# Optimization experiments

Measured on AMD Instinct MI355X. Metric: run time of the kernel, lower is better.

## Reference

```python
import jax, jax.numpy as jnp
import numpy as np

B, C, H, W = 8, 64, 64, 64   # C == embed_dim
NUM_EMBED = 8192
BETA = 0.25


def setup_inputs() -> dict:
    key = jax.random.key(0)
    k1, k2 = jax.random.split(key)
    z = jax.random.normal(k1, (B, C, H, W), dtype=jnp.float32)
    # nn.Embedding init: uniform(-1/num_embed, 1/num_embed)
    embedding = jax.random.uniform(
        k2, (NUM_EMBED, C), minval=-1.0 / NUM_EMBED, maxval=1.0 / NUM_EMBED,
        dtype=jnp.float32)
    return {"z": z, "embedding": embedding}


def reference(z, embedding):
    beta = BETA
    num_embed, embed_dim = embedding.shape
    eps = 1e-10

    zc = jnp.transpose(z, (0, 2, 3, 1))            # b h w c
    zf = zc.reshape(-1, embed_dim)                 # [N, d]

    # cosine distance: normalize both (z detached in torch; argmax is
    # non-differentiable anyway)
    zn = jax.lax.stop_gradient(
        zf / jnp.linalg.norm(zf, axis=1, keepdims=True))
    en = embedding / jnp.linalg.norm(embedding, axis=1, keepdims=True)
    d = jnp.einsum('bd,nd->bn', zn, en)            # [N, K] similarity

    # sort(dim=1) then take last column == argmax
    encoding_indices = jnp.argmax(d, axis=1)       # [N]

    # one-hot @ codebook == gather (same math)
    z_q = jnp.take(embedding, encoding_indices, axis=0).reshape(zc.shape)

    sg = jax.lax.stop_gradient
    loss = beta * jnp.mean((sg(z_q) - zc) ** 2) + jnp.mean((z_q - sg(zc)) ** 2)

    # straight-through estimator, back to b c h w
    z_q_st = zc + sg(z_q - zc)
    out = jnp.transpose(z_q_st, (0, 3, 1, 2))

    # perplexity from one-hot usage histogram
    n_tok = encoding_indices.shape[0]
    avg_probs = jnp.zeros((num_embed,), dtype=d.dtype).at[encoding_indices].add(1.0) / n_tok
    perplexity = jnp.exp(-jnp.sum(avg_probs * jnp.log(avg_probs + eps)))

    idx_map = encoding_indices.reshape(z.shape[0], 1, z.shape[2], z.shape[3])
    return out, loss, perplexity, idx_map
```

## Files before the change

kernel.cpp:

```cpp
#include <hip/hip_runtime.h>
#include <hip/hip_bf16.h>
#include <math.h>

#define B_    8
#define C_    64
#define H_    64
#define W_    64
#define NUM_EMBED 8192
#define DIMS  64
#define N_TOK (B_ * H_ * W_)
#define N_ELEM (B_ * C_ * H_ * W_)

typedef short v8s __attribute__((ext_vector_type(8)));
typedef float v4f __attribute__((ext_vector_type(4)));

#define MARGIN 0.011f

__device__ __forceinline__ short bf16_rne(float x) {
    unsigned u = __float_as_uint(x);
    unsigned r = (u + 0x7FFFu + ((u >> 16) & 1u)) >> 16;
    return (short)r;
}
__device__ __forceinline__ unsigned mono(float f) {
    int b = __float_as_int(f);
    return (unsigned)(b ^ ((b >> 31) | 0x80000000));
}
__device__ __forceinline__ float demono(unsigned u) {
    int b = (u >> 31) ? (int)(u ^ 0x80000000u) : (int)~u;
    return __int_as_float(b);
}
__device__ __forceinline__ unsigned long long pack_win(float d, int code) {
    return ((unsigned long long)mono(d) << 32) | (unsigned)(0xFFFFFFFFu - (unsigned)code);
}

__global__ void invnorm_kernel(const float* __restrict__ emb, float* __restrict__ invn) {
    int wave = threadIdx.x >> 6;
    int lane = threadIdx.x & 63;
    int row  = blockIdx.x * 4 + wave;
    float v = emb[row * DIMS + lane];
    float s = v * v;
    #pragma unroll
    for (int off = 1; off < 64; off <<= 1) s += __shfl_xor(s, off, 64);
    if (lane == 0) invn[row] = 1.0f / sqrtf(s);
}

__global__ void en_frag_kernel(const float* __restrict__ emb, const float* __restrict__ invn,
                               v8s* __restrict__ ef) {
    int ch = blockIdx.x * 256 + threadIdx.x;
    int l  = ch & 63;
    int st = (ch >> 6) & 1;
    int ct = ch >> 7;
    int code = ct * 16 + (l & 15);
    int kb   = st * 32 + ((l >> 4) & 3) * 8;
    float rn = invn[code];
    v8s o;
    #pragma unroll
    for (int j = 0; j < 8; ++j) o[j] = bf16_rne(emb[code * DIMS + kb + j] * rn);
    ef[ch] = o;
}

__global__ __launch_bounds__(256)
void z_prep_kernel(const float* __restrict__ z, float* __restrict__ z_tok,
                   v8s* __restrict__ af) {
    __shared__ float zs[64][65];
    __shared__ float part[4][64];
    __shared__ float rn[64];
    const int tid = threadIdx.x;
    const int w   = tid & 63;
    const int cg  = tid >> 6;
    const int bh  = blockIdx.x;
    const int b   = bh >> 6, h = bh & 63;

    const float* zb = z + (size_t)b * (C_ * H_ * W_) + h * W_;
    float ss = 0.f;
    #pragma unroll
    for (int cc = 0; cc < 16; ++cc) {
        int c = cg * 16 + cc;
        float v = zb[c * (H_ * W_) + w];
        zs[c][w] = v;
        ss += v * v;
    }
    part[cg][w] = ss;
    __syncthreads();
    if (tid < 64) {
        float s = part[0][tid] + part[1][tid] + part[2][tid] + part[3][tid];
        rn[tid] = 1.0f / sqrtf(s);
    }
    __syncthreads();

    {
        int c  = tid & 63;
        int tg = tid >> 6;
        #pragma unroll
        for (int i = 0; i < 16; ++i) {
            int tloc = tg * 16 + i;
            z_tok[(size_t)(bh * 64 + tloc) * DIMS + c] = zs[c][tloc];
        }
    }
    #pragma unroll
    for (int ii = 0; ii < 2; ++ii) {
        int ch  = tid + ii * 256;
        int mtl = ch >> 7;
        int st  = (ch >> 6) & 1;
        int l   = ch & 63;
        int tloc = mtl * 16 + (l & 15);
        int kb   = st * 32 + ((l >> 4) & 3) * 8;
        float rr = rn[tloc];
        v8s o;
        #pragma unroll
        for (int j = 0; j < 8; ++j) o[j] = bf16_rne(zs[kb + j][tloc] * rr);
        af[(size_t)((bh * 4 + mtl) * 2 + st) * 64 + l] = o;
    }
}

#define RT 4
#define CHUNK_TILES 16
#define TILES_PER_BLOCK 64
#define CHUNKS (TILES_PER_BLOCK / CHUNK_TILES)

__global__ __launch_bounds__(512, 4)
void pass1_kernel(const v8s* __restrict__ af, const v8s* __restrict__ ef,
                  unsigned* __restrict__ tokmax) {
    __shared__ v8s lds[CHUNK_TILES * 2 * 64];
    const int tid  = threadIdx.x;
    const int lane = tid & 63;
    const int wave = tid >> 6;
    const int bm    = blockIdx.x >> 3;
    const int split = blockIdx.x & 7;
    const int tile0 = split * TILES_PER_BLOCK;

    const int mtb = bm * 32 + wave * RT;
    v8s a[RT][2];
    #pragma unroll
    for (int r = 0; r < RT; ++r)
        #pragma unroll
        for (int s = 0; s < 2; ++s)
            a[r][s] = af[(size_t)((mtb + r) * 2 + s) * 64 + lane];

    v4f mx[RT];
    #pragma unroll
    for (int r = 0; r < RT; ++r) mx[r] = (v4f){-1e30f, -1e30f, -1e30f, -1e30f};

    const float4* gsrc = (const float4*)(ef + (size_t)tile0 * 2 * 64);
    float4* lf = (float4*)lds;
    float4 pre[4];
    #pragma unroll
    for (int i = 0; i < 4; ++i) pre[i] = gsrc[tid + i * 512];

    for (int c = 0; c < CHUNKS; ++c) {
        __syncthreads();
        #pragma unroll
        for (int i = 0; i < 4; ++i) lf[tid + i * 512] = pre[i];
        if (c + 1 < CHUNKS) {
            const float4* nx = gsrc + (size_t)(c + 1) * 2048;
            #pragma unroll
            for (int i = 0; i < 4; ++i) pre[i] = nx[tid + i * 512];
        }
        __syncthreads();
        #pragma unroll
        for (int j = 0; j < CHUNK_TILES; ++j) {
            v8s b0 = lds[(j * 2 + 0) * 64 + lane];
            v8s b1 = lds[(j * 2 + 1) * 64 + lane];
            #pragma unroll
            for (int r = 0; r < RT; ++r) {
                v4f t = (v4f){0.f, 0.f, 0.f, 0.f};
                t = __builtin_amdgcn_mfma_f32_16x16x32_bf16(a[r][0], b0, t, 0, 0, 0);
                t = __builtin_amdgcn_mfma_f32_16x16x32_bf16(a[r][1], b1, t, 0, 0, 0);
                mx[r][0] = fmaxf(mx[r][0], t[0]);
                mx[r][1] = fmaxf(mx[r][1], t[1]);
                mx[r][2] = fmaxf(mx[r][2], t[2]);
                mx[r][3] = fmaxf(mx[r][3], t[3]);
            }
        }
    }
    #pragma unroll
    for (int r = 0; r < RT; ++r)
        #pragma unroll
        for (int i = 0; i < 4; ++i) {
            float v = mx[r][i];
            v = fmaxf(v, __shfl_xor(v, 1, 64));
            v = fmaxf(v, __shfl_xor(v, 2, 64));
            v = fmaxf(v, __shfl_xor(v, 4, 64));
            v = fmaxf(v, __shfl_xor(v, 8, 64));
            mx[r][i] = v;
        }
    if ((lane & 15) == 0) {
        int q = lane >> 4;
        #pragma unroll
        for (int r = 0; r < RT; ++r)
            #pragma unroll
            for (int i = 0; i < 4; ++i) {
                int tok = (mtb + r) * 16 + q * 4 + i;
                atomicMax(&tokmax[tok], mono(mx[r][i]));
            }
    }
}

__global__ __launch_bounds__(512, 4)
void pass2_kernel(const v8s* __restrict__ af, const v8s* __restrict__ ef,
                  const unsigned* __restrict__ tokmax,
                  const float* __restrict__ z_tok, const float* __restrict__ emb,
                  const float* __restrict__ invn,
                  unsigned long long* __restrict__ winner) {
    __shared__ v8s lds[CHUNK_TILES * 2 * 64];
    const int tid  = threadIdx.x;
    const int lane = tid & 63;
    const int wave = tid >> 6;
    const int bm    = blockIdx.x >> 3;
    const int split = blockIdx.x & 7;
    const int tile0 = split * TILES_PER_BLOCK;

    const int mtb = bm * 32 + wave * RT;
    v8s a[RT][2];
    #pragma unroll
    for (int r = 0; r < RT; ++r)
        #pragma unroll
        for (int s = 0; s < 2; ++s)
            a[r][s] = af[(size_t)((mtb + r) * 2 + s) * 64 + lane];

    float thr[RT][4];
    {
        int q = lane >> 4;
        #pragma unroll
        for (int r = 0; r < RT; ++r)
            #pragma unroll
            for (int i = 0; i < 4; ++i)
                thr[r][i] = demono(tokmax[(mtb + r) * 16 + q * 4 + i]) - MARGIN;
    }

    const float4* gsrc = (const float4*)(ef + (size_t)tile0 * 2 * 64);
    float4* lf = (float4*)lds;
    float4 pre[4];
    #pragma unroll
    for (int i = 0; i < 4; ++i) pre[i] = gsrc[tid + i * 512];

    for (int c = 0; c < CHUNKS; ++c) {
        __syncthreads();
        #pragma unroll
        for (int i = 0; i < 4; ++i) lf[tid + i * 512] = pre[i];
        if (c + 1 < CHUNKS) {
            const float4* nx = gsrc + (size_t)(c + 1) * 2048;
            #pragma unroll
            for (int i = 0; i < 4; ++i) pre[i] = nx[tid + i * 512];
        }
        __syncthreads();
        #pragma unroll 4
        for (int j = 0; j < CHUNK_TILES; ++j) {
            v8s b0 = lds[(j * 2 + 0) * 64 + lane];
            v8s b1 = lds[(j * 2 + 1) * 64 + lane];
            v4f acc[RT];
            #pragma unroll
            for (int r = 0; r < RT; ++r) {
                v4f t = (v4f){0.f, 0.f, 0.f, 0.f};
                t = __builtin_amdgcn_mfma_f32_16x16x32_bf16(a[r][0], b0, t, 0, 0, 0);
                t = __builtin_amdgcn_mfma_f32_16x16x32_bf16(a[r][1], b1, t, 0, 0, 0);
                acc[r] = t;
            }
            unsigned pm = 0;
            #pragma unroll
            for (int r = 0; r < RT; ++r)
                #pragma unroll
                for (int i = 0; i < 4; ++i)
                    if (acc[r][i] >= thr[r][i]) pm |= (1u << (r * 4 + i));
            unsigned long long act = __ballot(pm != 0);
            if (act) {
                const int ctile = tile0 + c * CHUNK_TILES + j;
                while (act) {
                    int sl = __ffsll(act) - 1;
                    act &= act - 1;
                    unsigned lm = __shfl(pm, sl, 64);
                    const int code = ctile * 16 + (sl & 15);
                    while (lm) {
                        int bit = __ffs(lm) - 1;
                        lm &= lm - 1;
                        int r = bit >> 2, i = bit & 3;
                        int tok = (mtb + r) * 16 + ((sl >> 4) & 3) * 4 + i;
                        float p = z_tok[(size_t)tok * DIMS + lane] *
                                  emb[(size_t)code * DIMS + lane];
                        #pragma unroll
                        for (int o = 32; o; o >>= 1) p += __shfl_xor(p, o, 64);
                        float d = p * invn[code];
                        if (lane == 0) atomicMax(&winner[tok], pack_win(d, code));
                    }
                }
            }
        }
    }
}

__global__ void fin_idx_kernel(const unsigned long long* __restrict__ winner,
                               int* __restrict__ idx, float* __restrict__ idxmap) {
    int t = blockIdx.x * 256 + threadIdx.x;
    unsigned code = 0xFFFFFFFFu - (unsigned)(winner[t] & 0xFFFFFFFFull);
    idx[t] = (int)code;
    idxmap[t] = (float)code;
}

__global__ void gather_loss_kernel(const float* __restrict__ z,
                                   const float* __restrict__ emb,
                                   const int* __restrict__ idx,
                                   float* __restrict__ out,
                                   float* __restrict__ partial,
                                   int* __restrict__ hist) {
    __shared__ float red[256];
    const int tid  = threadIdx.x;
    const int lane = tid & 63;
    const int wave = tid >> 6;
    const int bt   = blockIdx.x;
    const int b    = bt >> 6;
    const int h    = bt & 63;

    const int t  = bt * 64 + lane;
    const int id = idx[t];
    const long base = (long)b * (C_ * H_ * W_) + h * W_ + lane;

    float sse = 0.f;
    #pragma unroll
    for (int cc = 0; cc < 16; ++cc) {
        const int c = wave * 16 + cc;
        const float q  = emb[id * DIMS + c];
        const float zv = z[base + (long)c * (H_ * W_)];
        out[base + (long)c * (H_ * W_)] = zv + (q - zv);
        const float d = q - zv;
        sse += d * d;
    }

    red[tid] = sse;
    __syncthreads();
    for (int s = 128; s > 0; s >>= 1) {
        if (tid < s) red[tid] += red[tid + s];
        __syncthreads();
    }
    if (tid == 0) partial[bt] = red[0];
    if (wave == 0) atomicAdd(&hist[id], 1);
}

__global__ void finalize_kernel(const float* __restrict__ partial,
                                const int* __restrict__ hist,
                                float* __restrict__ out_scal) {
    __shared__ double red[256];
    const int tid = threadIdx.x;

    double s = 0.0;
    for (int i = tid; i < 512; i += 256) s += (double)partial[i];
    red[tid] = s;
    __syncthreads();
    for (int st = 128; st > 0; st >>= 1) {
        if (tid < st) red[tid] += red[tid + st];
        __syncthreads();
    }
    const double sse = red[0];
    __syncthreads();

    double e = 0.0;
    for (int k = tid; k < NUM_EMBED; k += 256) {
        float p = (float)hist[k] / (float)N_TOK;
        e += (double)(p * logf(p + 1e-10f));
    }
    red[tid] = e;
    __syncthreads();
    for (int st = 128; st > 0; st >>= 1) {
        if (tid < st) red[tid] += red[tid + st];
        __syncthreads();
    }
    if (tid == 0) {
        out_scal[0] = (float)(1.25 * sse / (double)N_ELEM);
        out_scal[1] = expf(-(float)red[0]);
    }
}

extern "C" void kernel_launch(void* const* d_in, const int* in_sizes, int n_in,
                              void* d_out, int out_size, void* d_ws, size_t ws_size,
                              hipStream_t stream) {
    const float* z   = (const float*)d_in[0];
    const float* emb = (const float*)d_in[1];
    float* o = (float*)d_out;

    char* ws = (char*)d_ws;
    v8s*  af      = (v8s*)ws;
    v8s*  ef      = (v8s*)(ws + 4194304);
    unsigned long long* winner = (unsigned long long*)(ws + 5242880);
    unsigned* tokmax = (unsigned*)(ws + 5505024);
    int*   idx     = (int*)(ws + 5636096);
    float* invn    = (float*)(ws + 5767168);
    int*   hist    = (int*)(ws + 5799936);
    float* partial = (float*)(ws + 5832704);

    float* out_q      = o;
    float* out_scal   = o + N_ELEM;
    float* out_idxmap = o + N_ELEM + 2;
    float* z_tok      = o;

    hipMemsetAsync(tokmax, 0, N_TOK * sizeof(unsigned), stream);
    hipMemsetAsync(winner, 0, N_TOK * sizeof(unsigned long long), stream);
    hipMemsetAsync(hist,   0, NUM_EMBED * sizeof(int), stream);

    invnorm_kernel<<<NUM_EMBED / 4, 256, 0, stream>>>(emb, invn);
    en_frag_kernel<<<256, 256, 0, stream>>>(emb, invn, ef);
    z_prep_kernel<<<512, 256, 0, stream>>>(z, z_tok, af);
    pass1_kernel<<<512, 512, 0, stream>>>(af, ef, tokmax);
    pass2_kernel<<<512, 512, 0, stream>>>(af, ef, tokmax, z_tok, emb, invn, winner);
    fin_idx_kernel<<<N_TOK / 256, 256, 0, stream>>>(winner, idx, out_idxmap);
    gather_loss_kernel<<<N_TOK / 64, 256, 0, stream>>>(z, emb, idx, out_q, partial, hist);
    finalize_kernel<<<1, 256, 0, stream>>>(partial, hist, out_scal);
}
```

Baseline: 196.1 us.

## Replace second MFMA pass with per-chunk max bounds and fp32 chunk rescoring

Pass1 now records a rounded-up 16-bit per-chunk maximum similarity for every token across 32 codebook chunks of 256 codes, plus the global max. The second full MFMA sweep over the codebook is replaced by a per-token rescore kernel. It rescans in fp32 only the chunks whose upper bound reaches the threshold, then does an in-wave argmax with lowest-index tie-breaking. This removes a full second GEMM pass, the 64-bit atomics and the finalize-index kernel. The cost is extra cmax writes and scattered fp32 codebook reads for every chunk that qualifies.

```diff
diff --git a/kernel.cpp b/kernel.cpp
--- a/kernel.cpp
+++ b/kernel.cpp
@@ -28,9 +28,6 @@
 __device__ __forceinline__ float demono(unsigned u) {
     int b = (u >> 31) ? (int)(u ^ 0x80000000u) : (int)~u;
     return __int_as_float(b);
-}
-__device__ __forceinline__ unsigned long long pack_win(float d, int code) {
-    return ((unsigned long long)mono(d) << 32) | (unsigned)(0xFFFFFFFFu - (unsigned)code);
 }
 
 __global__ void invnorm_kernel(const float* __restrict__ emb, float* __restrict__ invn) {
@@ -117,10 +114,12 @@
 #define CHUNK_TILES 16
 #define TILES_PER_BLOCK 64
 #define CHUNKS (TILES_PER_BLOCK / CHUNK_TILES)
+#define NCHUNK_TOT 32
 
 __global__ __launch_bounds__(512, 4)
 void pass1_kernel(const v8s* __restrict__ af, const v8s* __restrict__ ef,
-                  unsigned* __restrict__ tokmax) {
+                  unsigned* __restrict__ tokmax,
+                  unsigned short* __restrict__ cmax) {
     __shared__ v8s lds[CHUNK_TILES * 2 * 64];
     const int tid  = threadIdx.x;
     const int lane = tid & 63;
@@ -137,9 +136,9 @@
         for (int s = 0; s < 2; ++s)
             a[r][s] = af[(size_t)((mtb + r) * 2 + s) * 64 + lane];
 
-    v4f mx[RT];
-    #pragma unroll
-    for (int r = 0; r < RT; ++r) mx[r] = (v4f){-1e30f, -1e30f, -1e30f, -1e30f};
+    v4f gm[RT];
+    #pragma unroll
+    for (int r = 0; r < RT; ++r) gm[r] = (v4f){-1e30f, -1e30f, -1e30f, -1e30f};
 
     const float4* gsrc = (const float4*)(ef + (size_t)tile0 * 2 * 64);
     float4* lf = (float4*)lds;
@@ -157,6 +156,11 @@
             for (int i = 0; i < 4; ++i) pre[i] = nx[tid + i * 512];
         }
         __syncthreads();
+
+        v4f mxc[RT];
+        #pragma unroll
+        for (int r = 0; r < RT; ++r) mxc[r] = (v4f){-1e30f, -1e30f, -1e30f, -1e30f};
+
         #pragma unroll
         for (int j = 0; j < CHUNK_TILES; ++j) {
             v8s b0 = lds[(j * 2 + 0) * 64 + lane];
@@ -166,24 +170,39 @@
                 v4f t = (v4f){0.f, 0.f, 0.f, 0.f};
                 t = __builtin_amdgcn_mfma_f32_16x16x32_bf16(a[r][0], b0, t, 0, 0, 0);
                 t = __builtin_amdgcn_mfma_f32_16x16x32_bf16(a[r][1], b1, t, 0, 0, 0);
-                mx[r][0] = fmaxf(mx[r][0], t[0]);
-                mx[r][1] = fmaxf(mx[r][1], t[1]);
-                mx[r][2] = fmaxf(mx[r][2], t[2]);
-                mx[r][3] = fmaxf(mx[r][3], t[3]);
+                mxc[r][0] = fmaxf(mxc[r][0], t[0]);
+                mxc[r][1] = fmaxf(mxc[r][1], t[1]);
+                mxc[r][2] = fmaxf(mxc[r][2], t[2]);
+                mxc[r][3] = fmaxf(mxc[r][3], t[3]);
             }
         }
-    }
-    #pragma unroll
-    for (int r = 0; r < RT; ++r)
-        #pragma unroll
-        for (int i = 0; i < 4; ++i) {
-            float v = mx[r][i];
-            v = fmaxf(v, __shfl_xor(v, 1, 64));
-            v = fmaxf(v, __shfl_xor(v, 2, 64));
-            v = fmaxf(v, __shfl_xor(v, 4, 64));
-            v = fmaxf(v, __shfl_xor(v, 8, 64));
-            mx[r][i] = v;
-        }
+
+        #pragma unroll
+        for (int r = 0; r < RT; ++r)
+            #pragma unroll
+            for (int i = 0; i < 4; ++i) {
+                float v = mxc[r][i];
+                v = fmaxf(v, __shfl_xor(v, 1, 64));
+                v = fmaxf(v, __shfl_xor(v, 2, 64));
+                v = fmaxf(v, __shfl_xor(v, 4, 64));
+                v = fmaxf(v, __shfl_xor(v, 8, 64));
+                mxc[r][i] = v;
+                gm[r][i]  = fmaxf(gm[r][i], v);
+            }
+        if ((lane & 15) == 0) {
+            const int q   = lane >> 4;
+            const int cid = split * CHUNKS + c;
+            #pragma unroll
+            for (int r = 0; r < RT; ++r)
+                #pragma unroll
+                for (int i = 0; i < 4; ++i) {
+                    int tok = (mtb + r) * 16 + q * 4 + i;
+                    cmax[tok * NCHUNK_TOT + cid] =
+                        (unsigned short)((mono(mxc[r][i]) + 0xFFFFu) >> 16);
+                }
+        }
+    }
+
     if ((lane & 15) == 0) {
         int q = lane >> 4;
         #pragma unroll
@@ -191,109 +210,76 @@
             #pragma unroll
             for (int i = 0; i < 4; ++i) {
                 int tok = (mtb + r) * 16 + q * 4 + i;
-                atomicMax(&tokmax[tok], mono(mx[r][i]));
+                atomicMax(&tokmax[tok], mono(gm[r][i]));
             }
     }
 }
 
-__global__ __launch_bounds__(512, 4)
-void pass2_kernel(const v8s* __restrict__ af, const v8s* __restrict__ ef,
-                  const unsigned* __restrict__ tokmax,
-                  const float* __restrict__ z_tok, const float* __restrict__ emb,
-                  const float* __restrict__ invn,
-                  unsigned long long* __restrict__ winner) {
-    __shared__ v8s lds[CHUNK_TILES * 2 * 64];
-    const int tid  = threadIdx.x;
-    const int lane = tid & 63;
-    const int wave = tid >> 6;
-    const int bm    = blockIdx.x >> 3;
-    const int split = blockIdx.x & 7;
-    const int tile0 = split * TILES_PER_BLOCK;
-
-    const int mtb = bm * 32 + wave * RT;
-    v8s a[RT][2];
-    #pragma unroll
-    for (int r = 0; r < RT; ++r)
-        #pragma unroll
-        for (int s = 0; s < 2; ++s)
-            a[r][s] = af[(size_t)((mtb + r) * 2 + s) * 64 + lane];
-
-    float thr[RT][4];
+__global__ __launch_bounds__(256)
+void rescore_kernel(const unsigned short* __restrict__ cmax,
+                    const unsigned* __restrict__ tokmax,
+                    const float* __restrict__ z_tok,
+                    const float* __restrict__ emb,
+                    const float* __restrict__ invn,
+                    int* __restrict__ idx, float* __restrict__ idxmap) {
+    __shared__ float zsh[4][64];
+    const int tid   = threadIdx.x;
+    const int lane  = tid & 63;
+    const int wave  = tid >> 6;
+    const int token = blockIdx.x * 4 + wave;
+
+    zsh[wave][lane] = z_tok[(size_t)token * DIMS + lane];
+    __syncthreads();
+
+    float4 zr[16];
     {
-        int q = lane >> 4;
-        #pragma unroll
-        for (int r = 0; r < RT; ++r)
-            #pragma unroll
-            for (int i = 0; i < 4; ++i)
-                thr[r][i] = demono(tokmax[(mtb + r) * 16 + q * 4 + i]) - MARGIN;
-    }
-
-    const float4* gsrc = (const float4*)(ef + (size_t)tile0 * 2 * 64);
-    float4* lf = (float4*)lds;
-    float4 pre[4];
-    #pragma unroll
-    for (int i = 0; i < 4; ++i) pre[i] = gsrc[tid + i * 512];
-
-    for (int c = 0; c < CHUNKS; ++c) {
-        __syncthreads();
-        #pragma unroll
-        for (int i = 0; i < 4; ++i) lf[tid + i * 512] = pre[i];
-        if (c + 1 < CHUNKS) {
-            const float4* nx = gsrc + (size_t)(c + 1) * 2048;
-            #pragma unroll
-            for (int i = 0; i < 4; ++i) pre[i] = nx[tid + i * 512];
-        }
-        __syncthreads();
-        #pragma unroll 4
-        for (int j = 0; j < CHUNK_TILES; ++j) {
-            v8s b0 = lds[(j * 2 + 0) * 64 + lane];
-            v8s b1 = lds[(j * 2 + 1) * 64 + lane];
-            v4f acc[RT];
-            #pragma unroll
-            for (int r = 0; r < RT; ++r) {
-                v4f t = (v4f){0.f, 0.f, 0.f, 0.f};
-                t = __builtin_amdgcn_mfma_f32_16x16x32_bf16(a[r][0], b0, t, 0, 0, 0);
-                t = __builtin_amdgcn_mfma_f32_16x16x32_bf16(a[r][1], b1, t, 0, 0, 0);
-                acc[r] = t;
+        const float4* zp = (const float4*)zsh[wave];
+        #pragma unroll
+        for (int i = 0; i < 16; ++i) zr[i] = zp[i];
+    }
+
+    const float thrf = demono(tokmax[token]) - MARGIN;
+    unsigned long long qual;
+    {
+        float ub = -1e30f;
+        if (lane < NCHUNK_TOT)
+            ub = demono(((unsigned)cmax[token * NCHUNK_TOT + lane]) << 16);
+        qual = __ballot(ub >= thrf);
+    }
+
+    float bv = -1e30f;
+    int   bc = 0x7FFFFFFF;
+    while (qual) {
+        const int cid = __ffsll(qual) - 1;
+        qual &= qual - 1;
+        const int base = cid * 256;
+        #pragma unroll
+        for (int k = 0; k < 4; ++k) {
+            const int code = base + k * 64 + lane;
+            const float4* ep = (const float4*)(emb + (size_t)code * DIMS);
+            float s = 0.f;
+            #pragma unroll
+            for (int i = 0; i < 16; ++i) {
+                float4 e = ep[i];
+                s = fmaf(zr[i].x, e.x, s);
+                s = fmaf(zr[i].y, e.y, s);
+                s = fmaf(zr[i].z, e.z, s);
+                s = fmaf(zr[i].w, e.w, s);
             }
-            unsigned pm = 0;
-            #pragma unroll
-            for (int r = 0; r < RT; ++r)
-                #pragma unroll
-                for (int i = 0; i < 4; ++i)
-                    if (acc[r][i] >= thr[r][i]) pm |= (1u << (r * 4 + i));
-            unsigned long long act = __ballot(pm != 0);
-            if (act) {
-                const int ctile = tile0 + c * CHUNK_TILES + j;
-                while (act) {
-                    int sl = __ffsll(act) - 1;
-                    act &= act - 1;
-                    unsigned lm = __shfl(pm, sl, 64);
-                    const int code = ctile * 16 + (sl & 15);
-                    while (lm) {
-                        int bit = __ffs(lm) - 1;
-                        lm &= lm - 1;
-                        int r = bit >> 2, i = bit & 3;
-                        int tok = (mtb + r) * 16 + ((sl >> 4) & 3) * 4 + i;
-                        float p = z_tok[(size_t)tok * DIMS + lane] *
-                                  emb[(size_t)code * DIMS + lane];
-                        #pragma unroll
-                        for (int o = 32; o; o >>= 1) p += __shfl_xor(p, o, 64);
-                        float d = p * invn[code];
-                        if (lane == 0) atomicMax(&winner[tok], pack_win(d, code));
-                    }
-                }
-            }
-        }
-    }
-}
-
-__global__ void fin_idx_kernel(const unsigned long long* __restrict__ winner,
-                               int* __restrict__ idx, float* __restrict__ idxmap) {
-    int t = blockIdx.x * 256 + threadIdx.x;
-    unsigned code = 0xFFFFFFFFu - (unsigned)(winner[t] & 0xFFFFFFFFull);
-    idx[t] = (int)code;
-    idxmap[t] = (float)code;
+            const float val = s * invn[code];
+            if (val > bv || (val == bv && code < bc)) { bv = val; bc = code; }
+        }
+    }
+    #pragma unroll
+    for (int off = 1; off < 64; off <<= 1) {
+        float ov = __shfl_xor(bv, off, 64);
+        int   oc = __shfl_xor(bc, off, 64);
+        if (ov > bv || (ov == bv && oc < bc)) { bv = ov; bc = oc; }
+    }
+    if (lane == 0) {
+        idx[token]    = bc;
+        idxmap[token] = (float)bc;
+    }
 }
 
 __global__ void gather_loss_kernel(const float* __restrict__ z,
@@ -379,12 +365,12 @@
     char* ws = (char*)d_ws;
     v8s*  af      = (v8s*)ws;
     v8s*  ef      = (v8s*)(ws + 4194304);
-    unsigned long long* winner = (unsigned long long*)(ws + 5242880);
-    unsigned* tokmax = (unsigned*)(ws + 5505024);
-    int*   idx     = (int*)(ws + 5636096);
-    float* invn    = (float*)(ws + 5767168);
-    int*   hist    = (int*)(ws + 5799936);
-    float* partial = (float*)(ws + 5832704);
+    unsigned short* cmaxb = (unsigned short*)(ws + 5242880);
+    unsigned* tokmax = (unsigned*)(ws + 7340032);
+    int*   idx     = (int*)(ws + 7471104);
+    float* invn    = (float*)(ws + 7602176);
+    int*   hist    = (int*)(ws + 7634944);
+    float* partial = (float*)(ws + 7667712);
 
     float* out_q      = o;
     float* out_scal   = o + N_ELEM;
@@ -392,15 +378,14 @@
     float* z_tok      = o;
 
     hipMemsetAsync(tokmax, 0, N_TOK * sizeof(unsigned), stream);
-    hipMemsetAsync(winner, 0, N_TOK * sizeof(unsigned long long), stream);
     hipMemsetAsync(hist,   0, NUM_EMBED * sizeof(int), stream);
 
     invnorm_kernel<<<NUM_EMBED / 4, 256, 0, stream>>>(emb, invn);
     en_frag_kernel<<<256, 256, 0, stream>>>(emb, invn, ef);
     z_prep_kernel<<<512, 256, 0, stream>>>(z, z_tok, af);
-    pass1_kernel<<<512, 512, 0, stream>>>(af, ef, tokmax);
-    pass2_kernel<<<512, 512, 0, stream>>>(af, ef, tokmax, z_tok, emb, invn, winner);
-    fin_idx_kernel<<<N_TOK / 256, 256, 0, stream>>>(winner, idx, out_idxmap);
+    pass1_kernel<<<512, 512, 0, stream>>>(af, ef, tokmax, cmaxb);
+    rescore_kernel<<<N_TOK / 4, 256, 0, stream>>>(cmaxb, tokmax, z_tok, emb, invn,
+                                                  idx, out_idxmap);
     gather_loss_kernel<<<N_TOK / 64, 256, 0, stream>>>(z, emb, idx, out_q, partial, hist);
     finalize_kernel<<<1, 256, 0, stream>>>(partial, hist, out_scal);
 }
```

New measurement: 590.0 us. 201% more time.
